# Performance work log

Hardware: AMD Instinct MI355X
Metric: run time of the kernel (lower is better)

The kernel has to match this reference:

```python
import jax, jax.numpy as jnp
import numpy as np

N = 8192
D = 2048      # input_dim
DH = 1024     # input_dim // r
DO = 1024     # output_dim

def setup_inputs() -> dict:
    key = jax.random.key(0)
    ks = jax.random.split(key, 11)
    s_in = 1.0 / np.sqrt(D)
    s_h = 1.0 / np.sqrt(DH)
    return {
        "O0": jax.random.normal(ks[0], (N, D), dtype=jnp.float32),
        "Ww": jax.random.uniform(ks[1], (DH, D), jnp.float32, -s_in, s_in),
        "Wb": jax.random.uniform(ks[2], (DH,), jnp.float32, -s_in, s_in),
        "Uw": jax.random.uniform(ks[3], (DH, D), jnp.float32, -s_in, s_in),
        "Ub": jax.random.uniform(ks[4], (DH,), jnp.float32, -s_in, s_in),
        "Hw": jax.random.uniform(ks[5], (DH, D), jnp.float32, -s_in, s_in),
        "Hb": jax.random.uniform(ks[6], (DH,), jnp.float32, -s_in, s_in),
        "fc0w": jax.random.uniform(ks[7], (D, DH), jnp.float32, -s_h, s_h),
        "fc0b": jax.random.uniform(ks[8], (D,), jnp.float32, -s_h, s_h),
        "fc1w": jax.random.uniform(ks[9], (DO, D), jnp.float32, -s_in, s_in),
        "fc1b": jax.random.uniform(ks[10], (DO,), jnp.float32, -s_in, s_in),
    }

def reference(O0, Ww, Wb, Uw, Ub, Hw, Hb, fc0w, fc0b, fc1w, fc1b):
    q = O0 @ Ww.T + Wb              # [N, DH]
    k = O0 @ Uw.T + Ub              # [N, DH]
    v = O0 @ Hw.T + Hb              # [N, DH]
    scores = q @ k.T                # [N, N], unscaled as in the original
    R1 = jax.nn.softmax(scores, axis=1)
    ctx = R1 @ v                    # [N, DH]
    O1 = O0 + (ctx @ fc0w.T + fc0b) # residual, [N, D]
    O2 = O1 @ fc1w.T + fc1b         # [N, DO]
    return (O1, O2)
```

## Files before the change

### kernel.cpp

```cpp
#include <hip/hip_runtime.h>
#include <cstdint>
#include <cstddef>

typedef _Float16 f16;
typedef _Float16 f16x8 __attribute__((ext_vector_type(8)));
typedef _Float16 f16x4 __attribute__((ext_vector_type(4)));
typedef float    f32x4 __attribute__((ext_vector_type(4)));

#define BM 128
#define BN 128
#define BK 64

__global__ __launch_bounds__(256) void cvt_f32_f16(const float* __restrict__ in,
                                                   f16* __restrict__ out, int n) {
  int i = (blockIdx.x * 256 + threadIdx.x) * 4;
  if (i < n) {
    float4 v = *(const float4*)(in + i);
    f16x4 h; h[0] = (f16)v.x; h[1] = (f16)v.y; h[2] = (f16)v.z; h[3] = (f16)v.w;
    *(f16x4*)(out + i) = h;
  }
}

__global__ __launch_bounds__(256) void transpose_f16(const f16* __restrict__ in,
                                                     f16* __restrict__ out,
                                                     int R, int C) {
  __shared__ f16 tile[64][65];
  const int r0 = blockIdx.y * 64, c0 = blockIdx.x * 64;
  const int t = threadIdx.x;
#pragma unroll
  for (int p = 0; p < 2; p++) {
    int s = t + p * 256;
    int r = s >> 3, q = s & 7;
    f16x8 v = *(const f16x8*)(in + (size_t)(r0 + r) * C + c0 + q * 8);
#pragma unroll
    for (int e = 0; e < 8; e++) tile[r][q * 8 + e] = v[e];
  }
  __syncthreads();
#pragma unroll
  for (int p = 0; p < 2; p++) {
    int s = t + p * 256;
    int r = s >> 3, q = s & 7;
    f16x8 v;
#pragma unroll
    for (int e = 0; e < 8; e++) v[e] = tile[q * 8 + e][r];
    *(f16x8*)(out + (size_t)(c0 + r) * R + r0 + q * 8) = v;
  }
}

template <int MODE>
__global__ __launch_bounds__(256) void gemm_bt(
    const f16* __restrict__ A, const f16* __restrict__ B,
    int M, int N, int K, int lda, int ldb,
    const float* __restrict__ bias,
    f16* __restrict__ outH, int ldo,
    float* __restrict__ stats, int sld,
    const float* __restrict__ resid, int ldr,
    float* __restrict__ outF, int ldof) {
  __shared__ f16 lA[BM * BK];
  __shared__ f16 lB[BN * BK];
  const int t = threadIdx.x;
  const int bn = blockIdx.x, bm = blockIdx.y;
  const int m0 = bm * BM, n0 = bn * BN;
  const int wave = t >> 6, lane = t & 63;
  const int wr = wave >> 1, wc = wave & 1;
  const int quad = lane >> 4, l16 = lane & 15;

  const int rc = lane >> 3;
  const int kcs = (lane & 7) ^ rc;
  const f16* gA = A + (size_t)(m0 + rc) * lda + kcs * 8;
  const f16* gB = B + (size_t)(n0 + rc) * ldb + kcs * 8;

  f32x4 acc[4][4];
#pragma unroll
  for (int i = 0; i < 4; i++)
#pragma unroll
    for (int j = 0; j < 4; j++)
#pragma unroll
      for (int e = 0; e < 4; e++) acc[i][j][e] = 0.0f;

  const int nk = K / BK;
  for (int kt = 0; kt < nk; ++kt) {
#pragma unroll
    for (int j = 0; j < 4; j++) {
      const int c = wave * 4 + j;
      __builtin_amdgcn_global_load_lds(
          (const __attribute__((address_space(1))) void*)(gA + (size_t)c * 8 * lda),
          (__attribute__((address_space(3))) void*)(lA + c * 512), 16, 0, 0);
    }
#pragma unroll
    for (int j = 0; j < 4; j++) {
      const int c = wave * 4 + j;
      __builtin_amdgcn_global_load_lds(
          (const __attribute__((address_space(1))) void*)(gB + (size_t)c * 8 * ldb),
          (__attribute__((address_space(3))) void*)(lB + c * 512), 16, 0, 0);
    }
    gA += BK; gB += BK;
    __syncthreads();

    f16x8 af[2][4], bf[2][4];
#pragma unroll
    for (int h = 0; h < 2; h++) {
      const int p = ((h * 4 + quad) ^ (l16 & 7)) * 8;
#pragma unroll
      for (int i = 0; i < 4; i++)
        af[h][i] = *(const f16x8*)(lA + (wr * 64 + i * 16 + l16) * 64 + p);
#pragma unroll
      for (int j = 0; j < 4; j++)
        bf[h][j] = *(const f16x8*)(lB + (wc * 64 + j * 16 + l16) * 64 + p);
    }
#pragma unroll
    for (int h = 0; h < 2; h++)
#pragma unroll
      for (int i = 0; i < 4; i++)
#pragma unroll
        for (int j = 0; j < 4; j++)
          acc[i][j] = __builtin_amdgcn_mfma_f32_16x16x32_f16(af[h][i], bf[h][j],
                                                             acc[i][j], 0, 0, 0);
    __syncthreads();
  }

  const int mrow = m0 + wr * 64;
  const int ncol = n0 + wc * 64;
  float bv[4];
  if constexpr (MODE == 0 || MODE == 3 || MODE == 4) {
#pragma unroll
    for (int j = 0; j < 4; j++) bv[j] = bias[ncol + j * 16 + l16];
  }
#pragma unroll
  for (int fi = 0; fi < 4; fi++) {
#pragma unroll
    for (int i = 0; i < 4; i++) {
      const int gr = mrow + fi * 16 + quad * 4 + i;
      if constexpr (MODE == 1) {
        float mx = acc[fi][0][i];
        mx = fmaxf(mx, acc[fi][1][i]);
        mx = fmaxf(mx, acc[fi][2][i]);
        mx = fmaxf(mx, acc[fi][3][i]);
        mx = fmaxf(mx, __shfl_xor(mx, 1));
        mx = fmaxf(mx, __shfl_xor(mx, 2));
        mx = fmaxf(mx, __shfl_xor(mx, 4));
        mx = fmaxf(mx, __shfl_xor(mx, 8));
        if (l16 == 0) stats[(size_t)gr * sld + (blockIdx.x * 2 + wc)] = mx;
#pragma unroll
        for (int fj = 0; fj < 4; fj++) {
          const int gc = ncol + fj * 16 + l16;
          outH[(size_t)gr * ldo + gc] = (f16)(acc[fi][fj][i] - mx);
        }
      } else {
#pragma unroll
        for (int fj = 0; fj < 4; fj++) {
          const int gc = ncol + fj * 16 + l16;
          float v = acc[fi][fj][i];
          if constexpr (MODE == 0) outH[(size_t)gr * ldo + gc] = (f16)(v + bv[fj]);
          if constexpr (MODE == 2) outH[(size_t)gr * ldo + gc] = (f16)v;
          if constexpr (MODE == 3) {
            float o = v + bv[fj] + resid[(size_t)gr * ldr + gc];
            outF[(size_t)gr * ldof + gc] = o;
            outH[(size_t)gr * ldo + gc] = (f16)o;
          }
          if constexpr (MODE == 4) outF[(size_t)gr * ldof + gc] = v + bv[fj];
        }
      }
    }
  }
}

__global__ __launch_bounds__(256) void softmax_row(f16* __restrict__ S,
                                                   const float* __restrict__ stats,
                                                   int N, int sld) {
  const int row = blockIdx.x;
  const int t = threadIdx.x;
  __shared__ float sm[128];
  __shared__ float red[4];
  if (t < 128) sm[t] = stats[(size_t)row * sld + t];
  __syncthreads();
  float m = -1e30f;
#pragma unroll 16
  for (int i = 0; i < 128; i++) m = fmaxf(m, sm[i]);

  f16* rp = S + (size_t)row * N + t * 32;
  const float d = sm[t >> 1] - m;
  float ev[32];
  float sum = 0.0f;
#pragma unroll
  for (int v8 = 0; v8 < 4; v8++) {
    f16x8 v = *(f16x8*)(rp + v8 * 8);
#pragma unroll
    for (int e = 0; e < 8; e++) {
      float x = (float)v[e] + d;
      float ex = __expf(x);
      ev[v8 * 8 + e] = ex;
      sum += ex;
    }
  }
#pragma unroll
  for (int off = 32; off > 0; off >>= 1) sum += __shfl_down(sum, off);
  if ((t & 63) == 0) red[t >> 6] = sum;
  __syncthreads();
  const float rl = 1.0f / (red[0] + red[1] + red[2] + red[3]);
#pragma unroll
  for (int v8 = 0; v8 < 4; v8++) {
    f16x8 v;
#pragma unroll
    for (int e = 0; e < 8; e++) v[e] = (f16)(ev[v8 * 8 + e] * rl);
    *(f16x8*)(rp + v8 * 8) = v;
  }
}

extern "C" void kernel_launch(void* const* d_in, const int* in_sizes, int n_in,
                              void* d_out, int out_size, void* d_ws, size_t ws_size,
                              hipStream_t stream) {
  const float* O0   = (const float*)d_in[0];
  const float* Ww   = (const float*)d_in[1];
  const float* Wb   = (const float*)d_in[2];
  const float* Uw   = (const float*)d_in[3];
  const float* Ub   = (const float*)d_in[4];
  const float* Hw   = (const float*)d_in[5];
  const float* Hb   = (const float*)d_in[6];
  const float* fc0w = (const float*)d_in[7];
  const float* fc0b = (const float*)d_in[8];
  const float* fc1w = (const float*)d_in[9];
  const float* fc1b = (const float*)d_in[10];

  const int N = 8192, D = 2048, DH = 1024, DO = 1024;

  char* w = (char*)d_ws;
  f16* Wwh   = (f16*)w; w += (size_t)DH * D * 2;
  f16* Uwh   = (f16*)w; w += (size_t)DH * D * 2;
  f16* Hwh   = (f16*)w; w += (size_t)DH * D * 2;
  f16* fc0wh = (f16*)w; w += (size_t)D * DH * 2;
  f16* fc1wh = (f16*)w; w += (size_t)DO * D * 2;
  f16* ctxh  = (f16*)w; w += (size_t)N * DH * 2;
  float* stats = (float*)w; w += (size_t)N * 128 * 4;
  f16* Sb    = (f16*)w;

  f16* oh  = (f16*)d_out;
  f16* qh  = oh;
  f16* kh  = oh + (size_t)N * DH;
  f16* vT  = oh + (size_t)2 * N * DH;
  f16* O0h = oh + (size_t)3 * N * DH;
  f16* vtmp = Sb;
  f16* O1h  = Sb;

  {
    int n = DH * D;
    int grid = n / 1024;
    cvt_f32_f16<<<grid, 256, 0, stream>>>(Ww, Wwh, n);
    cvt_f32_f16<<<grid, 256, 0, stream>>>(Uw, Uwh, n);
    cvt_f32_f16<<<grid, 256, 0, stream>>>(Hw, Hwh, n);
    cvt_f32_f16<<<grid, 256, 0, stream>>>(fc0w, fc0wh, n);
    cvt_f32_f16<<<grid, 256, 0, stream>>>(fc1w, fc1wh, n);
    int n0 = N * D;
    cvt_f32_f16<<<n0 / 1024, 256, 0, stream>>>(O0, O0h, n0);
  }

  {
    dim3 g(DH / BN, N / BM);
    gemm_bt<0><<<g, 256, 0, stream>>>(O0h, Wwh, N, DH, D, D, D, Wb,
                                      qh, DH, nullptr, 0, nullptr, 0, nullptr, 0);
    gemm_bt<0><<<g, 256, 0, stream>>>(O0h, Uwh, N, DH, D, D, D, Ub,
                                      kh, DH, nullptr, 0, nullptr, 0, nullptr, 0);
    gemm_bt<0><<<g, 256, 0, stream>>>(O0h, Hwh, N, DH, D, D, D, Hb,
                                      vtmp, DH, nullptr, 0, nullptr, 0, nullptr, 0);
  }

  transpose_f16<<<dim3(DH / 64, N / 64), 256, 0, stream>>>(vtmp, vT, N, DH);

  gemm_bt<1><<<dim3(N / BN, N / BM), 256, 0, stream>>>(
      qh, kh, N, N, DH, DH, DH, nullptr, Sb, N, stats, 128, nullptr, 0, nullptr, 0);

  softmax_row<<<N, 256, 0, stream>>>(Sb, stats, N, 128);

  gemm_bt<2><<<dim3(DH / BN, N / BM), 256, 0, stream>>>(
      Sb, vT, N, DH, N, N, N, nullptr, ctxh, DH, nullptr, 0, nullptr, 0, nullptr, 0);

  gemm_bt<3><<<dim3(D / BN, N / BM), 256, 0, stream>>>(
      ctxh, fc0wh, N, D, DH, DH, DH, fc0b, O1h, D, nullptr, 0,
      O0, D, (float*)d_out, D);

  gemm_bt<4><<<dim3(DO / BN, N / BM), 256, 0, stream>>>(
      O1h, fc1wh, N, DO, D, D, D, fc1b, nullptr, 0, nullptr, 0,
      nullptr, 0, (float*)d_out + (size_t)N * D, DO);
}
```

Baseline: 888.9 us.

## Fuse Q/K/V projections into one GEMM with concatenated weights and bias

Replaces the three separate Q, K and V projection GEMMs with a single GEMM of width 3*DH. It relies on Ww, Uw and Hw being converted into contiguous fp16 buffers, and copies the three biases into one concatenated buffer. The interleaved QKV output is then read with a stride of 3*DH by the score GEMM and by the V transpose. The GEMM address arithmetic also moves to 32-bit byte offsets with a wave-uniform readfirstlane index, and the epilogue stores are unrolled. The goal is fewer launches and better machine fill on the projection step, at the cost of strided Q/K reads.

```diff
diff --git a/kernel.cpp b/kernel.cpp
--- a/kernel.cpp
+++ b/kernel.cpp
@@ -22,6 +22,7 @@
 }
 
 __global__ __launch_bounds__(256) void transpose_f16(const f16* __restrict__ in,
+                                                     int ldi,
                                                      f16* __restrict__ out,
                                                      int R, int C) {
   __shared__ f16 tile[64][65];
@@ -31,7 +32,7 @@
   for (int p = 0; p < 2; p++) {
     int s = t + p * 256;
     int r = s >> 3, q = s & 7;
-    f16x8 v = *(const f16x8*)(in + (size_t)(r0 + r) * C + c0 + q * 8);
+    f16x8 v = *(const f16x8*)(in + (size_t)(r0 + r) * ldi + c0 + q * 8);
 #pragma unroll
     for (int e = 0; e < 8; e++) tile[r][q * 8 + e] = v[e];
   }
@@ -59,16 +60,18 @@
   __shared__ f16 lA[BM * BK];
   __shared__ f16 lB[BN * BK];
   const int t = threadIdx.x;
-  const int bn = blockIdx.x, bm = blockIdx.y;
-  const int m0 = bm * BM, n0 = bn * BN;
+  const int m0 = blockIdx.y * BM, n0 = blockIdx.x * BN;
   const int wave = t >> 6, lane = t & 63;
   const int wr = wave >> 1, wc = wave & 1;
   const int quad = lane >> 4, l16 = lane & 15;
 
   const int rc = lane >> 3;
   const int kcs = (lane & 7) ^ rc;
-  const f16* gA = A + (size_t)(m0 + rc) * lda + kcs * 8;
-  const f16* gB = B + (size_t)(n0 + rc) * ldb + kcs * 8;
+  const uint32_t offA = (uint32_t)(rc * lda + kcs * 8) * 2u;
+  const uint32_t offB = (uint32_t)(rc * ldb + kcs * 8) * 2u;
+  const char* bAp = (const char*)(A + (size_t)m0 * lda);
+  const char* bBp = (const char*)(B + (size_t)n0 * ldb);
+  const int wq = __builtin_amdgcn_readfirstlane(wave * 4);
 
   f32x4 acc[4][4];
 #pragma unroll
@@ -80,21 +83,19 @@
 
   const int nk = K / BK;
   for (int kt = 0; kt < nk; ++kt) {
+    const size_t kb = (size_t)(kt * BK) * 2;
 #pragma unroll
     for (int j = 0; j < 4; j++) {
-      const int c = wave * 4 + j;
+      const int c = wq + j;
       __builtin_amdgcn_global_load_lds(
-          (const __attribute__((address_space(1))) void*)(gA + (size_t)c * 8 * lda),
+          (const __attribute__((address_space(1))) void*)
+              (bAp + ((size_t)(c * 8) * lda * 2 + kb) + offA),
           (__attribute__((address_space(3))) void*)(lA + c * 512), 16, 0, 0);
-    }
-#pragma unroll
-    for (int j = 0; j < 4; j++) {
-      const int c = wave * 4 + j;
       __builtin_amdgcn_global_load_lds(
-          (const __attribute__((address_space(1))) void*)(gB + (size_t)c * 8 * ldb),
+          (const __attribute__((address_space(1))) void*)
+              (bBp + ((size_t)(c * 8) * ldb * 2 + kb) + offB),
           (__attribute__((address_space(3))) void*)(lB + c * 512), 16, 0, 0);
     }
-    gA += BK; gB += BK;
     __syncthreads();
 
     f16x8 af[2][4], bf[2][4];
@@ -132,34 +133,46 @@
     for (int i = 0; i < 4; i++) {
       const int gr = mrow + fi * 16 + quad * 4 + i;
       if constexpr (MODE == 1) {
-        float mx = acc[fi][0][i];
-        mx = fmaxf(mx, acc[fi][1][i]);
-        mx = fmaxf(mx, acc[fi][2][i]);
-        mx = fmaxf(mx, acc[fi][3][i]);
+        float mx = fmaxf(fmaxf(acc[fi][0][i], acc[fi][1][i]),
+                         fmaxf(acc[fi][2][i], acc[fi][3][i]));
         mx = fmaxf(mx, __shfl_xor(mx, 1));
         mx = fmaxf(mx, __shfl_xor(mx, 2));
         mx = fmaxf(mx, __shfl_xor(mx, 4));
         mx = fmaxf(mx, __shfl_xor(mx, 8));
         if (l16 == 0) stats[(size_t)gr * sld + (blockIdx.x * 2 + wc)] = mx;
-#pragma unroll
-        for (int fj = 0; fj < 4; fj++) {
-          const int gc = ncol + fj * 16 + l16;
-          outH[(size_t)gr * ldo + gc] = (f16)(acc[fi][fj][i] - mx);
-        }
+        f16* rp = outH + (size_t)gr * ldo + ncol + l16;
+        rp[0]  = (f16)(acc[fi][0][i] - mx);
+        rp[16] = (f16)(acc[fi][1][i] - mx);
+        rp[32] = (f16)(acc[fi][2][i] - mx);
+        rp[48] = (f16)(acc[fi][3][i] - mx);
+      } else if constexpr (MODE == 0) {
+        f16* rp = outH + (size_t)gr * ldo + ncol + l16;
+        rp[0]  = (f16)(acc[fi][0][i] + bv[0]);
+        rp[16] = (f16)(acc[fi][1][i] + bv[1]);
+        rp[32] = (f16)(acc[fi][2][i] + bv[2]);
+        rp[48] = (f16)(acc[fi][3][i] + bv[3]);
+      } else if constexpr (MODE == 2) {
+        f16* rp = outH + (size_t)gr * ldo + ncol + l16;
+        rp[0]  = (f16)acc[fi][0][i];
+        rp[16] = (f16)acc[fi][1][i];
+        rp[32] = (f16)acc[fi][2][i];
+        rp[48] = (f16)acc[fi][3][i];
+      } else if constexpr (MODE == 3) {
+        float* rf = outF + (size_t)gr * ldof + ncol + l16;
+        const float* rr = resid + (size_t)gr * ldr + ncol + l16;
+        f16* rh = outH + (size_t)gr * ldo + ncol + l16;
+        float o0 = acc[fi][0][i] + bv[0] + rr[0];
+        float o1 = acc[fi][1][i] + bv[1] + rr[16];
+        float o2 = acc[fi][2][i] + bv[2] + rr[32];
+        float o3 = acc[fi][3][i] + bv[3] + rr[48];
+        rf[0] = o0; rf[16] = o1; rf[32] = o2; rf[48] = o3;
+        rh[0] = (f16)o0; rh[16] = (f16)o1; rh[32] = (f16)o2; rh[48] = (f16)o3;
       } else {
-#pragma unroll
-        for (int fj = 0; fj < 4; fj++) {
-          const int gc = ncol + fj * 16 + l16;
-          float v = acc[fi][fj][i];
-          if constexpr (MODE == 0) outH[(size_t)gr * ldo + gc] = (f16)(v + bv[fj]);
-          if constexpr (MODE == 2) outH[(size_t)gr * ldo + gc] = (f16)v;
-          if constexpr (MODE == 3) {
-            float o = v + bv[fj] + resid[(size_t)gr * ldr + gc];
-            outF[(size_t)gr * ldof + gc] = o;
-            outH[(size_t)gr * ldo + gc] = (f16)o;
-          }
-          if constexpr (MODE == 4) outF[(size_t)gr * ldof + gc] = v + bv[fj];
-        }
+        float* rf = outF + (size_t)gr * ldof + ncol + l16;
+        rf[0]  = acc[fi][0][i] + bv[0];
+        rf[16] = acc[fi][1][i] + bv[1];
+        rf[32] = acc[fi][2][i] + bv[2];
+        rf[48] = acc[fi][3][i] + bv[3];
       }
     }
   }
@@ -223,6 +236,7 @@
   const float* fc1b = (const float*)d_in[10];
 
   const int N = 8192, D = 2048, DH = 1024, DO = 1024;
+  const int NQKV = 3 * DH;
 
   char* w = (char*)d_ws;
   f16* Wwh   = (f16*)w; w += (size_t)DH * D * 2;
@@ -232,14 +246,17 @@
   f16* fc1wh = (f16*)w; w += (size_t)DO * D * 2;
   f16* ctxh  = (f16*)w; w += (size_t)N * DH * 2;
   float* stats = (float*)w; w += (size_t)N * 128 * 4;
+  float* biasC = (float*)w; w += (size_t)NQKV * 4;
+  w = (char*)(((uintptr_t)w + 255) & ~(uintptr_t)255);
   f16* Sb    = (f16*)w;
 
-  f16* oh  = (f16*)d_out;
-  f16* qh  = oh;
-  f16* kh  = oh + (size_t)N * DH;
-  f16* vT  = oh + (size_t)2 * N * DH;
-  f16* O0h = oh + (size_t)3 * N * DH;
-  f16* vtmp = Sb;
+  f16* oh   = (f16*)d_out;
+  f16* qkv  = oh;
+  f16* qh   = qkv;
+  f16* kh   = qkv + DH;
+  f16* vh   = qkv + 2 * DH;
+  f16* O0h  = oh + (size_t)N * NQKV;
+  f16* vT   = O0h + (size_t)N * D;
   f16* O1h  = Sb;
 
   {
@@ -250,29 +267,27 @@
     cvt_f32_f16<<<grid, 256, 0, stream>>>(Hw, Hwh, n);
     cvt_f32_f16<<<grid, 256, 0, stream>>>(fc0w, fc0wh, n);
     cvt_f32_f16<<<grid, 256, 0, stream>>>(fc1w, fc1wh, n);
-    int n0 = N * D;
-    cvt_f32_f16<<<n0 / 1024, 256, 0, stream>>>(O0, O0h, n0);
-  }
-
-  {
-    dim3 g(DH / BN, N / BM);
-    gemm_bt<0><<<g, 256, 0, stream>>>(O0h, Wwh, N, DH, D, D, D, Wb,
-                                      qh, DH, nullptr, 0, nullptr, 0, nullptr, 0);
-    gemm_bt<0><<<g, 256, 0, stream>>>(O0h, Uwh, N, DH, D, D, D, Ub,
-                                      kh, DH, nullptr, 0, nullptr, 0, nullptr, 0);
-    gemm_bt<0><<<g, 256, 0, stream>>>(O0h, Hwh, N, DH, D, D, D, Hb,
-                                      vtmp, DH, nullptr, 0, nullptr, 0, nullptr, 0);
-  }
-
-  transpose_f16<<<dim3(DH / 64, N / 64), 256, 0, stream>>>(vtmp, vT, N, DH);
+    cvt_f32_f16<<<(N * D) / 1024, 256, 0, stream>>>(O0, O0h, N * D);
+    hipMemcpyAsync(biasC,          Wb, DH * 4, hipMemcpyDeviceToDevice, stream);
+    hipMemcpyAsync(biasC + DH,     Ub, DH * 4, hipMemcpyDeviceToDevice, stream);
+    hipMemcpyAsync(biasC + 2 * DH, Hb, DH * 4, hipMemcpyDeviceToDevice, stream);
+  }
+
+  gemm_bt<0><<<dim3(NQKV / BN, N / BM), 256, 0, stream>>>(
+      O0h, Wwh, N, NQKV, D, D, D, biasC,
+      qkv, NQKV, nullptr, 0, nullptr, 0, nullptr, 0);
+
+  transpose_f16<<<dim3(DH / 64, N / 64), 256, 0, stream>>>(vh, NQKV, vT, N, DH);
 
   gemm_bt<1><<<dim3(N / BN, N / BM), 256, 0, stream>>>(
-      qh, kh, N, N, DH, DH, DH, nullptr, Sb, N, stats, 128, nullptr, 0, nullptr, 0);
+      qh, kh, N, N, DH, NQKV, NQKV, nullptr, Sb, N, stats, 128,
+      nullptr, 0, nullptr, 0);
 
   softmax_row<<<N, 256, 0, stream>>>(Sb, stats, N, 128);
 
   gemm_bt<2><<<dim3(DH / BN, N / BM), 256, 0, stream>>>(
-      Sb, vT, N, DH, N, N, N, nullptr, ctxh, DH, nullptr, 0, nullptr, 0, nullptr, 0);
+      Sb, vT, N, DH, N, N, N, nullptr, ctxh, DH, nullptr, 0, nullptr, 0,
+      nullptr, 0);
 
   gemm_bt<3><<<dim3(D / BN, N / BM), 256, 0, stream>>>(
       ctxh, fc0wh, N, D, DH, DH, DH, fc0b, O1h, D, nullptr, 0,
```

Measured after the change: 862.9 us. -2.9%, faster.
